# Performance work log

Measured on AMD Instinct MI355X. Metric: run time of the kernel, lower is better.

The kernel has to match this reference:

```python
import jax, jax.numpy as jnp
import numpy as np

B, T, V, D, H, L, NFF, K = 16, 256, 30000, 512, 256, 2, 2, 20
# D = input_size = hidden_size (required by residual in FeedForwardNet); H = hidden_size//2 per LSTM direction


def _lstm_dir(x, Wih, Whh, b, reverse):
    # x: [B,T,Din]; Wih: [4H,Din]; Whh: [4H,H]; b: [4H] (b_ih + b_hh)
    Bq = x.shape[0]
    Hd = Whh.shape[1]
    if reverse:
        x = x[:, ::-1]
    xw = jnp.einsum('bti,gi->btg', x, Wih) + b  # [B,T,4H]

    def step(carry, xw_t):
        h, c = carry
        g = xw_t + h @ Whh.T
        i, f, gg, o = jnp.split(g, 4, axis=-1)  # torch gate order i,f,g,o
        c = jax.nn.sigmoid(f) * c + jax.nn.sigmoid(i) * jnp.tanh(gg)
        h = jax.nn.sigmoid(o) * jnp.tanh(c)
        return (h, c), h

    h0 = jnp.zeros((Bq, Hd), x.dtype)
    _, hs = jax.lax.scan(step, (h0, h0), jnp.swapaxes(xw, 0, 1))
    hs = jnp.swapaxes(hs, 0, 1)  # [B,T,H]
    if reverse:
        hs = hs[:, ::-1]
    return hs


def _bilstm(x, Wih, Whh, b):
    # Wih: [L,2,4H,Din], Whh: [L,2,4H,H], b: [L,2,4H]; Din = 2H = D for all layers
    h = x
    for l in range(L):
        fwd = _lstm_dir(h, Wih[l, 0], Whh[l, 0], b[l, 0], False)
        bwd = _lstm_dir(h, Wih[l, 1], Whh[l, 1], b[l, 1], True)
        h = jnp.concatenate([fwd, bwd], axis=-1)  # [B,T,2H]
    return h


def _viterbi(em, start, end, trans):
    # em: [B,T,K] emissions, full mask; torchcrf Viterbi decode
    Bq, Tq, Kq = em.shape
    score = start + em[:, 0]  # [B,K]

    def step(score, em_t):
        bs = score[:, :, None] + trans[None] + em_t[:, None, :]  # [B,K,K]
        return jnp.max(bs, axis=1), jnp.argmax(bs, axis=1)

    score, hist = jax.lax.scan(step, score, jnp.swapaxes(em[:, 1:], 0, 1))  # hist [T-1,B,K]
    best = jnp.argmax(score + end, axis=-1)  # [B]

    def back(tag, h_t):
        prev = jnp.take_along_axis(h_t, tag[:, None], axis=1)[:, 0]
        return prev, prev

    _, prevs = jax.lax.scan(back, best, hist, reverse=True)  # [T-1,B]
    return jnp.concatenate([prevs, best[None]], axis=0).T  # [B,T]


def setup_inputs() -> dict:
    key = jax.random.key(0)
    ks = jax.random.split(key, 16)
    s = 0.05
    inp = {
        'x': jax.random.randint(ks[0], (B, T), 0, V),
        'emb': jax.random.normal(ks[1], (V, D), jnp.float32) * s,
        'lstm_Wih': jax.random.normal(ks[2], (L, 2, 4 * H, D), jnp.float32) * s,
        'lstm_Whh': jax.random.normal(ks[3], (L, 2, 4 * H, H), jnp.float32) * s,
        'lstm_b': jax.random.normal(ks[4], (L, 2, 4 * H), jnp.float32) * s,
        'ff_W1': jax.random.normal(ks[5], (NFF, D, D), jnp.float32) * s,
        'ff_b1': jax.random.normal(ks[6], (NFF, D), jnp.float32) * s,
        'ff_W2': jax.random.normal(ks[7], (NFF, D, D), jnp.float32) * s,
        'ff_b2': jax.random.normal(ks[8], (NFF, D), jnp.float32) * s,
        'ffo_W': jax.random.normal(ks[9], (H, D), jnp.float32) * s,
        'ffo_b': jax.random.normal(ks[10], (H,), jnp.float32) * s,
        'out_W': jax.random.normal(ks[11], (K, H), jnp.float32) * s,
        'out_b': jax.random.normal(ks[12], (K,), jnp.float32) * s,
        'crf_start': jax.random.normal(ks[13], (K,), jnp.float32) * 0.1,
        'crf_end': jax.random.normal(ks[14], (K,), jnp.float32) * 0.1,
        'crf_trans': jax.random.normal(ks[15], (K, K), jnp.float32) * 0.1,
    }
    return inp


def reference(x, emb, lstm_Wih, lstm_Whh, lstm_b, ff_W1, ff_b1, ff_W2, ff_b2,
              ffo_W, ffo_b, out_W, out_b, crf_start, crf_end, crf_trans):
    h = emb[x]                       # [B,T,D] frozen embedding lookup
    h = _bilstm(h, lstm_Wih, lstm_Whh, lstm_b)  # [B,T,D] (2H == D)
    res = h
    for n in range(NFF):             # residual MLP stack (dropout = identity in eval)
        h = jax.nn.relu(h @ ff_W1[n].T + ff_b1[n]) @ ff_W2[n].T + ff_b2[n]
    h = h + res
    h = h @ ffo_W.T + ffo_b          # [B,T,H] FeedForwardNet.output
    em = h @ out_W.T + out_b         # [B,T,K] emissions
    tag = _viterbi(em, crf_start, crf_end, crf_trans)  # [B,T] int32
    return em, tag
```

## Files before the change

### kernel.cpp

```cpp
#include <hip/hip_runtime.h>
#include <hip/hip_bf16.h>
#include <stdint.h>

typedef unsigned short u16;
typedef unsigned int   u32;
typedef __attribute__((ext_vector_type(4))) float f32x4;
typedef __attribute__((ext_vector_type(8))) short bf16x8;

#define SENT 0xAAAAAAAAu

static __device__ __forceinline__ u16 f2bf(float x) {
  union { float f; u32 u; } v; v.f = x;
  u32 r = v.u + 0x7FFFu + ((v.u >> 16) & 1u);
  return (u16)(r >> 16);
}
static __device__ __forceinline__ float bf2f(u16 b) {
  union { u32 u; float f; } v; v.u = ((u32)b) << 16;
  return v.f;
}


__global__ void split_hl(const float* __restrict__ in, u16* __restrict__ hi,
                         u16* __restrict__ lo, int n) {
  int i = blockIdx.x * 256 + threadIdx.x;
  if (i < n) {
    float v = in[i];
    u16 h = f2bf(v);
    hi[i] = h;
    lo[i] = f2bf(v - bf2f(h));
  }
}

__global__ void embed_split(const int* __restrict__ x, const float* __restrict__ emb,
                            u16* __restrict__ hi, u16* __restrict__ lo) {
  int gid = blockIdx.x * 256 + threadIdx.x;
  int bt = gid >> 9, d = gid & 511;
  float v = emb[(size_t)x[bt] * 512 + d];
  u16 h = f2bf(v);
  hi[gid] = h;
  lo[gid] = f2bf(v - bf2f(h));
}

__global__ void fill_sent(u32* __restrict__ p, int n) {
  int i = blockIdx.x * 256 + threadIdx.x;
  if (i < n) p[i] = SENT;
}

__global__ void lstm_wpack(const float* __restrict__ Whh, u32* __restrict__ wp) {
  int tid = blockIdx.x * 256 + threadIdx.x;
  int dw   = tid & 3;
  int lane = (tid >> 2) & 63;
  int pass = (tid >> 8) & 1;
  int kt   = (tid >> 9) & 7;
  int w    = (tid >> 12) & 3;
  int q    = (tid >> 14) & 15;
  int d    = (tid >> 18) & 1;
  int lyr  = (tid >> 19) & 1;
  int row = w * 256 + q * 16 + (lane & 15);
  int k   = kt * 32 + (lane >> 4) * 8 + dw * 2;
  const float* src = Whh + (((size_t)(lyr * 2 + d) * 1024 + row) * 256);
  float w0 = src[k], w1 = src[k + 1];
  u16 h0 = f2bf(w0), h1 = f2bf(w1);
  u32 out;
  if (pass == 0) out = (u32)h0 | ((u32)h1 << 16);
  else {
    u16 l0 = f2bf(w0 - bf2f(h0)), l1 = f2bf(w1 - bf2f(h1));
    out = (u32)l0 | ((u32)l1 << 16);
  }
  wp[tid] = out;
}

__global__ void resadd_split(const float* __restrict__ a, const float* __restrict__ b,
                             u16* __restrict__ hi, u16* __restrict__ lo, int n) {
  int i = blockIdx.x * 256 + threadIdx.x;
  if (i < n) {
    float v = a[i] + b[i];
    u16 h = f2bf(v);
    hi[i] = h;
    lo[i] = f2bf(v - bf2f(h));
  }
}

template<int RELU, int WF32, int WHL>
__global__ __launch_bounds__(256) void gemm_x3(
    const u16* __restrict__ Ahi, const u16* __restrict__ Alo,
    const u16* __restrict__ Bhi, const u16* __restrict__ Blo,
    const float* __restrict__ bias,
    float* __restrict__ Cf, u16* __restrict__ Chi, u16* __restrict__ Clo,
    int M, int N, int Kd)
{
  __shared__ u16 As_hi[128][40], As_lo[128][40], Bs_hi[128][40], Bs_lo[128][40];
  int t = threadIdx.x;
  int bm = blockIdx.x * 128, bn = blockIdx.y * 128;
  int l = t & 63, wid = t >> 6;
  int wy = wid >> 1, wx = wid & 1;
  f32x4 acc[4][4];
#pragma unroll
  for (int i = 0; i < 4; i++)
#pragma unroll
    for (int j = 0; j < 4; j++) acc[i][j] = (f32x4){0.f, 0.f, 0.f, 0.f};

  for (int kt = 0; kt < Kd; kt += 32) {
    __syncthreads();
#pragma unroll
    for (int cc = 0; cc < 2; cc++) {
      int c = t + cc * 256;
      int row = c >> 2, k8 = (c & 3) << 3;
      *(uint4*)&As_hi[row][k8] = *(const uint4*)(Ahi + (size_t)(bm + row) * Kd + kt + k8);
      *(uint4*)&As_lo[row][k8] = *(const uint4*)(Alo + (size_t)(bm + row) * Kd + kt + k8);
      *(uint4*)&Bs_hi[row][k8] = *(const uint4*)(Bhi + (size_t)(bn + row) * Kd + kt + k8);
      *(uint4*)&Bs_lo[row][k8] = *(const uint4*)(Blo + (size_t)(bn + row) * Kd + kt + k8);
    }
    __syncthreads();
    bf16x8 bh[4], bl[4];
    int k8 = (l >> 4) << 3;
#pragma unroll
    for (int ni = 0; ni < 4; ni++) {
      int r = wx * 64 + ni * 16 + (l & 15);
      bh[ni] = *(const bf16x8*)&Bs_hi[r][k8];
      bl[ni] = *(const bf16x8*)&Bs_lo[r][k8];
    }
#pragma unroll
    for (int mi = 0; mi < 4; mi++) {
      int r = wy * 64 + mi * 16 + (l & 15);
      bf16x8 ah = *(const bf16x8*)&As_hi[r][k8];
      bf16x8 al = *(const bf16x8*)&As_lo[r][k8];
#pragma unroll
      for (int ni = 0; ni < 4; ni++) {
        acc[mi][ni] = __builtin_amdgcn_mfma_f32_16x16x32_bf16(ah, bh[ni], acc[mi][ni], 0, 0, 0);
        acc[mi][ni] = __builtin_amdgcn_mfma_f32_16x16x32_bf16(ah, bl[ni], acc[mi][ni], 0, 0, 0);
        acc[mi][ni] = __builtin_amdgcn_mfma_f32_16x16x32_bf16(al, bh[ni], acc[mi][ni], 0, 0, 0);
      }
    }
  }
#pragma unroll
  for (int ni = 0; ni < 4; ni++) {
    int col = bn + wx * 64 + ni * 16 + (l & 15);
    float bv = bias ? bias[col] : 0.f;
#pragma unroll
    for (int mi = 0; mi < 4; mi++) {
#pragma unroll
      for (int r = 0; r < 4; r++) {
        int row = bm + wy * 64 + mi * 16 + (l >> 4) * 4 + r;
        float v = acc[mi][ni][r] + bv;
        if (RELU) v = fmaxf(v, 0.f);
        size_t o = (size_t)row * N + col;
        if (WF32) Cf[o] = v;
        if (WHL) { u16 h = f2bf(v); Chi[o] = h; Clo[o] = f2bf(v - bf2f(h)); }
      }
    }
  }
}

__global__ __launch_bounds__(256, 1) void lstm_rec(
    const u32* __restrict__ wpack_l,
    const float* __restrict__ xw_f, const float* __restrict__ xw_b,
    u32* __restrict__ hex_l,
    u16* __restrict__ out_hi, u16* __restrict__ out_lo, float* __restrict__ out_f)
{
  int bid = blockIdx.x;
  int dir = bid >> 4, q = bid & 15;
  int tid = threadIdx.x;
  int l = tid & 63, w = tid >> 6;
  int b15 = l & 15, k4 = (l >> 4) * 4;
  const float* xw = dir ? xw_b : xw_f;
  u32* hexd = hex_l + (size_t)dir * (1u << 20);

  bf16x8 wfrag[8][2];
  {
    const u32* wb = wpack_l + (((size_t)(dir * 16 + q) * 4 + w) * 16) * 256;
#pragma unroll
    for (int kt = 0; kt < 8; kt++)
#pragma unroll
      for (int p = 0; p < 2; p++) {
        union { uint4 q4; bf16x8 v; } u;
        u.q4 = *(const uint4*)(wb + ((kt * 2 + p) * 64 + l) * 4);
        wfrag[kt][p] = u.v;
      }
  }

  __shared__ float gbuf[4][16][17];
  __shared__ u16 hbH[16][17], hbL[16][17];
  int gu = tid & 15, gb = tid >> 4;
  float c_state = 0.f;

  for (int s = 0; s < 256; s++) {
    int tpos = dir ? (255 - s) : s;
    int col = w * 256 + q * 16 + b15;
    float x0 = xw[((size_t)((k4 + 0) * 256 + tpos)) * 1024 + col];
    float x1 = xw[((size_t)((k4 + 1) * 256 + tpos)) * 1024 + col];
    float x2 = xw[((size_t)((k4 + 2) * 256 + tpos)) * 1024 + col];
    float x3 = xw[((size_t)((k4 + 3) * 256 + tpos)) * 1024 + col];
    f32x4 aH = {x0, x1, x2, x3};
    f32x4 aL1 = {0.f, 0.f, 0.f, 0.f};
    f32x4 aL2 = {0.f, 0.f, 0.f, 0.f};

    if (s > 0) {
      u32 adh[8][4], adl[8][4];
      const u32* ah = hexd + ((size_t)(s - 1) * 16 + b15) * 128;
      const u32* al = ah + (1u << 19);
      for (int it = 0; it < (1 << 22); ++it) {
        bool ok = true;
#pragma unroll
        for (int kt = 0; kt < 8; kt++)
#pragma unroll
          for (int d4 = 0; d4 < 4; d4++) {
            int idx = kt * 16 + k4 + d4;
            adh[kt][d4] = __hip_atomic_load(ah + idx, __ATOMIC_RELAXED, __HIP_MEMORY_SCOPE_AGENT);
            adl[kt][d4] = __hip_atomic_load(al + idx, __ATOMIC_RELAXED, __HIP_MEMORY_SCOPE_AGENT);
            ok = ok && (adh[kt][d4] != SENT) && (adl[kt][d4] != SENT);
          }
        if (__all(ok)) break;
      }
#pragma unroll
      for (int kt = 0; kt < 8; kt++) {
        union { u32 u[4]; bf16x8 v; } fh, fl;
#pragma unroll
        for (int d4 = 0; d4 < 4; d4++) { fh.u[d4] = adh[kt][d4]; fl.u[d4] = adl[kt][d4]; }
        aH  = __builtin_amdgcn_mfma_f32_16x16x32_bf16(fh.v, wfrag[kt][0], aH, 0, 0, 0);
        aL1 = __builtin_amdgcn_mfma_f32_16x16x32_bf16(fh.v, wfrag[kt][1], aL1, 0, 0, 0);
        aL2 = __builtin_amdgcn_mfma_f32_16x16x32_bf16(fl.v, wfrag[kt][0], aL2, 0, 0, 0);
      }
    }
#pragma unroll
    for (int r = 0; r < 4; r++)
      gbuf[w][b15][k4 + r] = aH[r] + aL1[r] + aL2[r];
    __syncthreads();

    float gi = gbuf[0][gu][gb], gf = gbuf[1][gu][gb];
    float gg = gbuf[2][gu][gb], go = gbuf[3][gu][gb];
    float si = 1.f / (1.f + __expf(-gi));
    float sf = 1.f / (1.f + __expf(-gf));
    float so = 1.f / (1.f + __expf(-go));
    float eg = __expf(2.f * gg);
    float tg = (eg - 1.f) / (eg + 1.f);
    c_state = sf * c_state + si * tg;
    float ec = __expf(2.f * c_state);
    float th = (ec - 1.f) / (ec + 1.f);
    float h = so * th;
    u16 hb = f2bf(h);
    u16 lb = f2bf(h - bf2f(hb));
    hbH[gu][gb] = hb;
    hbL[gu][gb] = lb;
    size_t oo = (((size_t)gb * 256 + tpos) * 512) + dir * 256 + q * 16 + gu;
    out_hi[oo] = hb;
    out_lo[oo] = lb;
    if (out_f) out_f[oo] = h;
    __syncthreads();

    {
      int t2 = tid & 127;
      int bb = t2 & 15, up = t2 >> 4;
      u32* dst = hexd + ((size_t)s * 16 + bb) * 128 + (q * 8 + up);
      if (tid < 128) {
        u32 bits = (u32)hbH[up * 2][bb] | ((u32)hbH[up * 2 + 1][bb] << 16);
        if (bits == SENT) bits ^= 1u;
        __hip_atomic_store(dst, bits, __ATOMIC_RELAXED, __HIP_MEMORY_SCOPE_AGENT);
      } else {
        u32 bits = (u32)hbL[up * 2][bb] | ((u32)hbL[up * 2 + 1][bb] << 16);
        if (bits == SENT) bits ^= 1u;
        __hip_atomic_store(dst + (1u << 19), bits, __ATOMIC_RELAXED, __HIP_MEMORY_SCOPE_AGENT);
      }
    }
  }
}

__global__ __launch_bounds__(256) void out_gemm(const float* __restrict__ h,
                                                const float* __restrict__ Wo,
                                                const float* __restrict__ bo,
                                                float* __restrict__ em)
{
  int t = threadIdx.x;
  if (t >= 160) return;
  int r = t / 20, j = t - r * 20;
  int bt = blockIdx.x * 8 + r;
  const float* hr = h + (size_t)bt * 256;
  const float* wr = Wo + j * 256;
  float acc = 0.f;
#pragma unroll 4
  for (int k = 0; k < 256; k++) acc += hr[k] * wr[k];
  em[(size_t)bt * 20 + j] = acc + bo[j];
}

__global__ __launch_bounds__(192) void viterbi(const float* __restrict__ em,
                                               const float* __restrict__ cstart,
                                               const float* __restrict__ cend,
                                               const float* __restrict__ ctrans,
                                               float* __restrict__ tago)
{
  __shared__ float sc[8][20];
  __shared__ float tl[400];
  __shared__ unsigned char hist[255][8][20];
  int t = threadIdx.x;
  for (int i = t; i < 400; i += 192) tl[i] = ctrans[i];
  int bl = t / 20, j = t - bl * 20;
  bool act = (t < 160);
  int b = blockIdx.x * 8 + bl;
  if (act) sc[bl][j] = cstart[j] + em[((size_t)b * 256) * 20 + j];
  __syncthreads();
  for (int step = 1; step < 256; step++) {
    float best = -1e30f; int bi = 0;
    if (act) {
      best = sc[bl][0] + tl[j]; bi = 0;
#pragma unroll
      for (int i = 1; i < 20; i++) {
        float v = sc[bl][i] + tl[i * 20 + j];
        if (v > best) { best = v; bi = i; }
      }
      hist[step - 1][bl][j] = (unsigned char)bi;
    }
    __syncthreads();
    if (act) sc[bl][j] = best + em[((size_t)b * 256 + step) * 20 + j];
    __syncthreads();
  }
  if (act && j == 0) {
    float best = sc[bl][0] + cend[0]; int bj = 0;
    for (int i = 1; i < 20; i++) {
      float v = sc[bl][i] + cend[i];
      if (v > best) { best = v; bj = i; }
    }
    int tag = bj;
    tago[(size_t)b * 256 + 255] = (float)tag;
    for (int step = 254; step >= 0; step--) {
      tag = hist[step][bl][tag];
      tago[(size_t)b * 256 + step] = (float)tag;
    }
  }
}

extern "C" void kernel_launch(void* const* d_in, const int* in_sizes, int n_in,
                              void* d_out, int out_size, void* d_ws, size_t ws_size,
                              hipStream_t stream)
{
  const int*   x   = (const int*)  d_in[0];
  const float* emb = (const float*)d_in[1];
  const float* Wih = (const float*)d_in[2];
  const float* Whh = (const float*)d_in[3];
  const float* lb  = (const float*)d_in[4];
  const float* fW1 = (const float*)d_in[5];
  const float* fb1 = (const float*)d_in[6];
  const float* fW2 = (const float*)d_in[7];
  const float* fb2 = (const float*)d_in[8];
  const float* foW = (const float*)d_in[9];
  const float* fob = (const float*)d_in[10];
  const float* oW  = (const float*)d_in[11];
  const float* ob  = (const float*)d_in[12];
  const float* cst = (const float*)d_in[13];
  const float* cen = (const float*)d_in[14];
  const float* ctr = (const float*)d_in[15];

  const size_t MB = 1u << 20;
  if (ws_size < 100 * MB) return;
  char* ws = (char*)d_ws;

  u16* embHi = (u16*)(ws + 0 * MB);
  u16* embLo = (u16*)(ws + 4 * MB);
  u16* l1Hi  = (u16*)(ws + 8 * MB);
  u16* l1Lo  = (u16*)(ws + 12 * MB);
  float* l2F = (float*)(ws + 16 * MB);
  u16* l2Hi  = (u16*)(ws + 24 * MB);
  u16* l2Lo  = (u16*)(ws + 28 * MB);
  float* xwF = (float*)(ws + 32 * MB);
  float* xwB = (float*)(ws + 48 * MB);
  u32* hexB  = (u32*)(ws + 64 * MB);
  u32* wpck  = (u32*)(ws + 80 * MB);
  u16* wihHi = (u16*)(ws + 84 * MB);
  u16* wihLo = (u16*)(ws + 88 * MB);
  u16* fw1Hi = (u16*)(ws + 92 * MB);
  u16* fw1Lo = (u16*)(ws + 93 * MB);
  u16* fw2Hi = (u16*)(ws + 94 * MB);
  u16* fw2Lo = (u16*)(ws + 95 * MB);
  u16* ffoHi = (u16*)(ws + 96 * MB);
  u16* ffoLo = (u16*)(ws + 96 * MB + 512 * 1024);
  u16* t1Hi = (u16*)xwF;
  u16* t1Lo = (u16*)((char*)xwF + 4 * MB);
  u16* t2Hi = (u16*)xwB;
  u16* t2Lo = (u16*)((char*)xwB + 4 * MB);
  float* h2F = (float*)((char*)xwB + 8 * MB);
  u16* sumHi = (u16*)((char*)xwF + 8 * MB);
  u16* sumLo = (u16*)((char*)xwF + 12 * MB);
  float* h256F = (float*)xwF;

  float* em   = (float*)d_out;
  float* tago = (float*)d_out + 81920;

  dim3 blk(256);

  split_hl<<<8192, blk, 0, stream>>>(Wih, wihHi, wihLo, 4 * 1024 * 512);
  split_hl<<<2048, blk, 0, stream>>>(fW1, fw1Hi, fw1Lo, 2 * 512 * 512);
  split_hl<<<2048, blk, 0, stream>>>(fW2, fw2Hi, fw2Lo, 2 * 512 * 512);
  split_hl<<<512,  blk, 0, stream>>>(foW, ffoHi, ffoLo, 256 * 512);
  lstm_wpack<<<4096, blk, 0, stream>>>(Whh, wpck);
  embed_split<<<8192, blk, 0, stream>>>(x, emb, embHi, embLo);
  fill_sent<<<16384, blk, 0, stream>>>(hexB, 4 * 1024 * 1024);

  gemm_x3<0,1,0><<<dim3(32, 8), blk, 0, stream>>>(embHi, embLo,
      wihHi + 0 * 524288, wihLo + 0 * 524288, lb + 0 * 1024,
      xwF, nullptr, nullptr, 4096, 1024, 512);
  gemm_x3<0,1,0><<<dim3(32, 8), blk, 0, stream>>>(embHi, embLo,
      wihHi + 1 * 524288, wihLo + 1 * 524288, lb + 1 * 1024,
      xwB, nullptr, nullptr, 4096, 1024, 512);
  lstm_rec<<<32, blk, 0, stream>>>(wpck, xwF, xwB, hexB, l1Hi, l1Lo, nullptr);

  gemm_x3<0,1,0><<<dim3(32, 8), blk, 0, stream>>>(l1Hi, l1Lo,
      wihHi + 2 * 524288, wihLo + 2 * 524288, lb + 2 * 1024,
      xwF, nullptr, nullptr, 4096, 1024, 512);
  gemm_x3<0,1,0><<<dim3(32, 8), blk, 0, stream>>>(l1Hi, l1Lo,
      wihHi + 3 * 524288, wihLo + 3 * 524288, lb + 3 * 1024,
      xwB, nullptr, nullptr, 4096, 1024, 512);
  lstm_rec<<<32, blk, 0, stream>>>(wpck + (1u << 19), xwF, xwB,
      hexB + (2u << 20), l2Hi, l2Lo, l2F);

  gemm_x3<1,0,1><<<dim3(32, 4), blk, 0, stream>>>(l2Hi, l2Lo,
      fw1Hi + 0, fw1Lo + 0, fb1 + 0, nullptr, t1Hi, t1Lo, 4096, 512, 512);
  gemm_x3<0,0,1><<<dim3(32, 4), blk, 0, stream>>>(t1Hi, t1Lo,
      fw2Hi + 0, fw2Lo + 0, fb2 + 0, nullptr, t2Hi, t2Lo, 4096, 512, 512);
  gemm_x3<1,0,1><<<dim3(32, 4), blk, 0, stream>>>(t2Hi, t2Lo,
      fw1Hi + 262144, fw1Lo + 262144, fb1 + 512, nullptr, t1Hi, t1Lo, 4096, 512, 512);
  gemm_x3<0,1,0><<<dim3(32, 4), blk, 0, stream>>>(t1Hi, t1Lo,
      fw2Hi + 262144, fw2Lo + 262144, fb2 + 512, h2F, nullptr, nullptr, 4096, 512, 512);
  resadd_split<<<8192, blk, 0, stream>>>(h2F, l2F, sumHi, sumLo, 4096 * 512);
  gemm_x3<0,1,0><<<dim3(32, 2), blk, 0, stream>>>(sumHi, sumLo,
      ffoHi, ffoLo, fob, h256F, nullptr, nullptr, 4096, 256, 512);

  out_gemm<<<512, blk, 0, stream>>>(h256F, oW, ob, em);
  viterbi<<<2, dim3(192), 0, stream>>>(em, cst, cen, ctr, tago);
}
```

Before: 6.240 ms.

## Run each LSTM direction in one workgroup with LDS-shared hidden state

Replaces the 32-block LSTM recurrence, which exchanged hidden state through global memory with sentinel polling across 16 blocks per direction, with one 1024-thread workgroup per direction. That workgroup keeps all recurrent weight fragments in registers and shares h through double-buffered, swizzled LDS, synchronised only by __syncthreads. The input-projection GEMM now writes xw in a swizzled layout so each wave loads its gate inputs as contiguous float4 vectors, and the sentinel fill kernel is dropped. The cost is that only 2 CUs do the recurrence, with high register pressure per thread (wf holds 64 bf16x8 vectors), instead of spreading the matrix work over 32 CUs.

Measured after the change: 12.82 ms. +105.4%, slower.

```diff
diff --git a/kernel.cpp b/kernel.cpp
--- a/kernel.cpp
+++ b/kernel.cpp
@@ -6,8 +6,6 @@
 typedef unsigned int   u32;
 typedef __attribute__((ext_vector_type(4))) float f32x4;
 typedef __attribute__((ext_vector_type(8))) short bf16x8;
-
-#define SENT 0xAAAAAAAAu
 
 static __device__ __forceinline__ u16 f2bf(float x) {
   union { float f; u32 u; } v; v.f = x;
@@ -41,22 +39,17 @@
   lo[gid] = f2bf(v - bf2f(h));
 }
 
-__global__ void fill_sent(u32* __restrict__ p, int n) {
-  int i = blockIdx.x * 256 + threadIdx.x;
-  if (i < n) p[i] = SENT;
-}
-
 __global__ void lstm_wpack(const float* __restrict__ Whh, u32* __restrict__ wp) {
   int tid = blockIdx.x * 256 + threadIdx.x;
   int dw   = tid & 3;
   int lane = (tid >> 2) & 63;
   int pass = (tid >> 8) & 1;
   int kt   = (tid >> 9) & 7;
-  int w    = (tid >> 12) & 3;
-  int q    = (tid >> 14) & 15;
+  int g    = (tid >> 12) & 3;
+  int W    = (tid >> 14) & 15;
   int d    = (tid >> 18) & 1;
   int lyr  = (tid >> 19) & 1;
-  int row = w * 256 + q * 16 + (lane & 15);
+  int row = g * 256 + W * 16 + (lane & 15);
   int k   = kt * 32 + (lane >> 4) * 8 + dw * 2;
   const float* src = Whh + (((size_t)(lyr * 2 + d) * 1024 + row) * 256);
   float w0 = src[k], w1 = src[k + 1];
@@ -81,7 +74,7 @@
   }
 }
 
-template<int RELU, int WF32, int WHL>
+template<int RELU, int WF32, int WHL, int XSWZ>
 __global__ __launch_bounds__(256) void gemm_x3(
     const u16* __restrict__ Ahi, const u16* __restrict__ Alo,
     const u16* __restrict__ Bhi, const u16* __restrict__ Blo,
@@ -144,124 +137,111 @@
         int row = bm + wy * 64 + mi * 16 + (l >> 4) * 4 + r;
         float v = acc[mi][ni][r] + bv;
         if (RELU) v = fmaxf(v, 0.f);
-        size_t o = (size_t)row * N + col;
-        if (WF32) Cf[o] = v;
-        if (WHL) { u16 h = f2bf(v); Chi[o] = h; Clo[o] = f2bf(v - bf2f(h)); }
+        if (XSWZ) {
+          int tt = row & 255, b = row >> 8;
+          int g = col >> 8, c8 = col & 255;
+          int Wv = c8 >> 4, uu = c8 & 15;
+          int lane = ((b >> 2) << 4) | uu;
+          size_t o = ((((size_t)tt * 16 + Wv) * 4 + g) * 64 + lane) * 4 + (b & 3);
+          Cf[o] = v;
+        } else {
+          size_t o = (size_t)row * N + col;
+          if (WF32) Cf[o] = v;
+          if (WHL) { u16 h = f2bf(v); Chi[o] = h; Clo[o] = f2bf(v - bf2f(h)); }
+        }
       }
     }
   }
 }
 
-__global__ __launch_bounds__(256, 1) void lstm_rec(
+__global__ __launch_bounds__(1024, 1) void lstm_rec2(
     const u32* __restrict__ wpack_l,
-    const float* __restrict__ xw_f, const float* __restrict__ xw_b,
-    u32* __restrict__ hex_l,
+    const float* __restrict__ xwsw_f, const float* __restrict__ xwsw_b,
     u16* __restrict__ out_hi, u16* __restrict__ out_lo, float* __restrict__ out_f)
 {
-  int bid = blockIdx.x;
-  int dir = bid >> 4, q = bid & 15;
+  int dir = blockIdx.x;
   int tid = threadIdx.x;
-  int l = tid & 63, w = tid >> 6;
-  int b15 = l & 15, k4 = (l >> 4) * 4;
-  const float* xw = dir ? xw_b : xw_f;
-  u32* hexd = hex_l + (size_t)dir * (1u << 20);
-
-  bf16x8 wfrag[8][2];
-  {
-    const u32* wb = wpack_l + (((size_t)(dir * 16 + q) * 4 + w) * 16) * 256;
+  int W = tid >> 6, l = tid & 63;
+  int bb  = l & 15;
+  int mb  = (l >> 4) * 4;
+  int wu  = W * 16 + (l & 15);
+  const float* xw = dir ? xwsw_b : xwsw_f;
+
+  bf16x8 wf[4][8][2];
+#pragma unroll
+  for (int g = 0; g < 4; g++) {
+    const u32* wb = wpack_l + (size_t)((dir * 16 + W) * 4 + g) * 4096;
 #pragma unroll
     for (int kt = 0; kt < 8; kt++)
 #pragma unroll
-      for (int p = 0; p < 2; p++) {
-        union { uint4 q4; bf16x8 v; } u;
-        u.q4 = *(const uint4*)(wb + ((kt * 2 + p) * 64 + l) * 4);
-        wfrag[kt][p] = u.v;
-      }
-  }
-
-  __shared__ float gbuf[4][16][17];
-  __shared__ u16 hbH[16][17], hbL[16][17];
-  int gu = tid & 15, gb = tid >> 4;
-  float c_state = 0.f;
+      for (int p = 0; p < 2; p++)
+        wf[g][kt][p] = *(const bf16x8*)(const void*)(wb + ((kt * 2 + p) * 64 + l) * 4);
+  }
+
+  __shared__ u16 hH[2][16][256];
+  __shared__ u16 hL[2][16][256];
+
+  f32x4 cst = (f32x4){0.f, 0.f, 0.f, 0.f};
 
   for (int s = 0; s < 256; s++) {
     int tpos = dir ? (255 - s) : s;
-    int col = w * 256 + q * 16 + b15;
-    float x0 = xw[((size_t)((k4 + 0) * 256 + tpos)) * 1024 + col];
-    float x1 = xw[((size_t)((k4 + 1) * 256 + tpos)) * 1024 + col];
-    float x2 = xw[((size_t)((k4 + 2) * 256 + tpos)) * 1024 + col];
-    float x3 = xw[((size_t)((k4 + 3) * 256 + tpos)) * 1024 + col];
-    f32x4 aH = {x0, x1, x2, x3};
-    f32x4 aL1 = {0.f, 0.f, 0.f, 0.f};
-    f32x4 aL2 = {0.f, 0.f, 0.f, 0.f};
+    int cb = s & 1, pb = cb ^ 1;
+
+    const float* xb = xw + ((size_t)tpos * 16 + W) * 1024;
+    f32x4 xwv[4];
+#pragma unroll
+    for (int g = 0; g < 4; g++)
+      xwv[g] = *(const f32x4*)(xb + g * 256 + l * 4);
+
+    f32x4 acc[4];
+#pragma unroll
+    for (int g = 0; g < 4; g++) acc[g] = (f32x4){0.f, 0.f, 0.f, 0.f};
 
     if (s > 0) {
-      u32 adh[8][4], adl[8][4];
-      const u32* ah = hexd + ((size_t)(s - 1) * 16 + b15) * 128;
-      const u32* al = ah + (1u << 19);
-      for (int it = 0; it < (1 << 22); ++it) {
-        bool ok = true;
-#pragma unroll
-        for (int kt = 0; kt < 8; kt++)
-#pragma unroll
-          for (int d4 = 0; d4 < 4; d4++) {
-            int idx = kt * 16 + k4 + d4;
-            adh[kt][d4] = __hip_atomic_load(ah + idx, __ATOMIC_RELAXED, __HIP_MEMORY_SCOPE_AGENT);
-            adl[kt][d4] = __hip_atomic_load(al + idx, __ATOMIC_RELAXED, __HIP_MEMORY_SCOPE_AGENT);
-            ok = ok && (adh[kt][d4] != SENT) && (adl[kt][d4] != SENT);
-          }
-        if (__all(ok)) break;
+#pragma unroll
+      for (int kt = 0; kt < 8; kt++) {
+        int bx = (((kt * 4 + (l >> 4)) ^ (bb & 7)) << 3);
+        bf16x8 ah = *(const bf16x8*)&hH[pb][bb][bx];
+        bf16x8 al = *(const bf16x8*)&hL[pb][bb][bx];
+#pragma unroll
+        for (int g = 0; g < 4; g++)
+          acc[g] = __builtin_amdgcn_mfma_f32_16x16x32_bf16(ah, wf[g][kt][0], acc[g], 0, 0, 0);
+#pragma unroll
+        for (int g = 0; g < 4; g++)
+          acc[g] = __builtin_amdgcn_mfma_f32_16x16x32_bf16(ah, wf[g][kt][1], acc[g], 0, 0, 0);
+#pragma unroll
+        for (int g = 0; g < 4; g++)
+          acc[g] = __builtin_amdgcn_mfma_f32_16x16x32_bf16(al, wf[g][kt][0], acc[g], 0, 0, 0);
       }
-#pragma unroll
-      for (int kt = 0; kt < 8; kt++) {
-        union { u32 u[4]; bf16x8 v; } fh, fl;
-#pragma unroll
-        for (int d4 = 0; d4 < 4; d4++) { fh.u[d4] = adh[kt][d4]; fl.u[d4] = adl[kt][d4]; }
-        aH  = __builtin_amdgcn_mfma_f32_16x16x32_bf16(fh.v, wfrag[kt][0], aH, 0, 0, 0);
-        aL1 = __builtin_amdgcn_mfma_f32_16x16x32_bf16(fh.v, wfrag[kt][1], aL1, 0, 0, 0);
-        aL2 = __builtin_amdgcn_mfma_f32_16x16x32_bf16(fl.v, wfrag[kt][0], aL2, 0, 0, 0);
-      }
-    }
-#pragma unroll
-    for (int r = 0; r < 4; r++)
-      gbuf[w][b15][k4 + r] = aH[r] + aL1[r] + aL2[r];
+    }
+
+#pragma unroll
+    for (int r = 0; r < 4; r++) {
+      float gi = acc[0][r] + xwv[0][r];
+      float gf = acc[1][r] + xwv[1][r];
+      float gg = acc[2][r] + xwv[2][r];
+      float go = acc[3][r] + xwv[3][r];
+      float si = 1.f / (1.f + __expf(-gi));
+      float sf = 1.f / (1.f + __expf(-gf));
+      float so = 1.f / (1.f + __expf(-go));
+      float tg = 1.f - 2.f / (__expf(2.f * gg) + 1.f);
+      float c = sf * cst[r] + si * tg;
+      cst[r] = c;
+      float th = 1.f - 2.f / (__expf(2.f * c) + 1.f);
+      float h = so * th;
+
+      u16 hb = f2bf(h);
+      u16 lb = f2bf(h - bf2f(hb));
+      int b = mb + r;
+      int idx = ((((wu >> 3) ^ (b & 7)) << 3)) + (wu & 7);
+      hH[cb][b][idx] = hb;
+      hL[cb][b][idx] = lb;
+      size_t oo = (((size_t)b * 256 + tpos) * 512) + dir * 256 + wu;
+      out_hi[oo] = hb;
+      out_lo[oo] = lb;
+      if (out_f) out_f[oo] = h;
+    }
     __syncthreads();
-
-    float gi = gbuf[0][gu][gb], gf = gbuf[1][gu][gb];
-    float gg = gbuf[2][gu][gb], go = gbuf[3][gu][gb];
-    float si = 1.f / (1.f + __expf(-gi));
-    float sf = 1.f / (1.f + __expf(-gf));
-    float so = 1.f / (1.f + __expf(-go));
-    float eg = __expf(2.f * gg);
-    float tg = (eg - 1.f) / (eg + 1.f);
-    c_state = sf * c_state + si * tg;
-    float ec = __expf(2.f * c_state);
-    float th = (ec - 1.f) / (ec + 1.f);
-    float h = so * th;
-    u16 hb = f2bf(h);
-    u16 lb = f2bf(h - bf2f(hb));
-    hbH[gu][gb] = hb;
-    hbL[gu][gb] = lb;
-    size_t oo = (((size_t)gb * 256 + tpos) * 512) + dir * 256 + q * 16 + gu;
-    out_hi[oo] = hb;
-    out_lo[oo] = lb;
-    if (out_f) out_f[oo] = h;
-    __syncthreads();
-
-    {
-      int t2 = tid & 127;
-      int bb = t2 & 15, up = t2 >> 4;
-      u32* dst = hexd + ((size_t)s * 16 + bb) * 128 + (q * 8 + up);
-      if (tid < 128) {
-        u32 bits = (u32)hbH[up * 2][bb] | ((u32)hbH[up * 2 + 1][bb] << 16);
-        if (bits == SENT) bits ^= 1u;
-        __hip_atomic_store(dst, bits, __ATOMIC_RELAXED, __HIP_MEMORY_SCOPE_AGENT);
-      } else {
-        u32 bits = (u32)hbL[up * 2][bb] | ((u32)hbL[up * 2 + 1][bb] << 16);
-        if (bits == SENT) bits ^= 1u;
-        __hip_atomic_store(dst + (1u << 19), bits, __ATOMIC_RELAXED, __HIP_MEMORY_SCOPE_AGENT);
-      }
-    }
   }
 }
 
@@ -362,7 +342,6 @@
   u16* l2Lo  = (u16*)(ws + 28 * MB);
   float* xwF = (float*)(ws + 32 * MB);
   float* xwB = (float*)(ws + 48 * MB);
-  u32* hexB  = (u32*)(ws + 64 * MB);
   u32* wpck  = (u32*)(ws + 80 * MB);
   u16* wihHi = (u16*)(ws + 84 * MB);
   u16* wihLo = (u16*)(ws + 88 * MB);
@@ -392,35 +371,34 @@
   split_hl<<<512,  blk, 0, stream>>>(foW, ffoHi, ffoLo, 256 * 512);
   lstm_wpack<<<4096, blk, 0, stream>>>(Whh, wpck);
   embed_split<<<8192, blk, 0, stream>>>(x, emb, embHi, embLo);
-  fill_sent<<<16384, blk, 0, stream>>>(hexB, 4 * 1024 * 1024);
-
-  gemm_x3<0,1,0><<<dim3(32, 8), blk, 0, stream>>>(embHi, embLo,
+
+  gemm_x3<0,1,0,1><<<dim3(32, 8), blk, 0, stream>>>(embHi, embLo,
       wihHi + 0 * 524288, wihLo + 0 * 524288, lb + 0 * 1024,
       xwF, nullptr, nullptr, 4096, 1024, 512);
-  gemm_x3<0,1,0><<<dim3(32, 8), blk, 0, stream>>>(embHi, embLo,
+  gemm_x3<0,1,0,1><<<dim3(32, 8), blk, 0, stream>>>(embHi, embLo,
       wihHi + 1 * 524288, wihLo + 1 * 524288, lb + 1 * 1024,
       xwB, nullptr, nullptr, 4096, 1024, 512);
-  lstm_rec<<<32, blk, 0, stream>>>(wpck, xwF, xwB, hexB, l1Hi, l1Lo, nullptr);
-
-  gemm_x3<0,1,0><<<dim3(32, 8), blk, 0, stream>>>(l1Hi, l1Lo,
+  lstm_rec2<<<2, dim3(1024), 0, stream>>>(wpck, xwF, xwB, l1Hi, l1Lo, nullptr);
+
+  gemm_x3<0,1,0,1><<<dim3(32, 8), blk, 0, stream>>>(l1Hi, l1Lo,
       wihHi + 2 * 524288, wihLo + 2 * 524288, lb + 2 * 1024,
       xwF, nullptr, nullptr, 4096, 1024, 512);
-  gemm_x3<0,1,0><<<dim3(32, 8), blk, 0, stream>>>(l1Hi, l1Lo,
+  gemm_x3<0,1,0,1><<<dim3(32, 8), blk, 0, stream>>>(l1Hi, l1Lo,
       wihHi + 3 * 524288, wihLo + 3 * 524288, lb + 3 * 1024,
       xwB, nullptr, nullptr, 4096, 1024, 512);
-  lstm_rec<<<32, blk, 0, stream>>>(wpck + (1u << 19), xwF, xwB,
-      hexB + (2u << 20), l2Hi, l2Lo, l2F);
-
-  gemm_x3<1,0,1><<<dim3(32, 4), blk, 0, stream>>>(l2Hi, l2Lo,
+  lstm_rec2<<<2, dim3(1024), 0, stream>>>(wpck + (1u << 19), xwF, xwB,
+      l2Hi, l2Lo, l2F);
+
+  gemm_x3<1,0,1,0><<<dim3(32, 4), blk, 0, stream>>>(l2Hi, l2Lo,
       fw1Hi + 0, fw1Lo + 0, fb1 + 0, nullptr, t1Hi, t1Lo, 4096, 512, 512);
-  gemm_x3<0,0,1><<<dim3(32, 4), blk, 0, stream>>>(t1Hi, t1Lo,
+  gemm_x3<0,0,1,0><<<dim3(32, 4), blk, 0, stream>>>(t1Hi, t1Lo,
       fw2Hi + 0, fw2Lo + 0, fb2 + 0, nullptr, t2Hi, t2Lo, 4096, 512, 512);
-  gemm_x3<1,0,1><<<dim3(32, 4), blk, 0, stream>>>(t2Hi, t2Lo,
+  gemm_x3<1,0,1,0><<<dim3(32, 4), blk, 0, stream>>>(t2Hi, t2Lo,
       fw1Hi + 262144, fw1Lo + 262144, fb1 + 512, nullptr, t1Hi, t1Lo, 4096, 512, 512);
-  gemm_x3<0,1,0><<<dim3(32, 4), blk, 0, stream>>>(t1Hi, t1Lo,
+  gemm_x3<0,1,0,0><<<dim3(32, 4), blk, 0, stream>>>(t1Hi, t1Lo,
       fw2Hi + 262144, fw2Lo + 262144, fb2 + 512, h2F, nullptr, nullptr, 4096, 512, 512);
   resadd_split<<<8192, blk, 0, stream>>>(h2F, l2F, sumHi, sumLo, 4096 * 512);
-  gemm_x3<0,1,0><<<dim3(32, 2), blk, 0, stream>>>(sumHi, sumLo,
+  gemm_x3<0,1,0,0><<<dim3(32, 2), blk, 0, stream>>>(sumHi, sumLo,
       ffoHi, ffoLo, fob, h256F, nullptr, nullptr, 4096, 256, 512);
 
   out_gemm<<<512, blk, 0, stream>>>(h256F, oW, ob, em);
```
